# Kernel optimization log

Measured on AMD Instinct MI355X. Metric: run time of the kernel, lower is better.

The kernel has to match this reference:

```python
import jax, jax.numpy as jnp
import numpy as np

N_NODES = 100000
N_EDGES = 3200000
IN_DIM = 64
N_SEQ = 8
HID1 = 256
HID2 = 128
END = 64
OUT = 1


def _glorot(key, shape):
    fan_in, fan_out = shape
    lim = (6.0 / (fan_in + fan_out)) ** 0.5
    return jax.random.uniform(key, shape, jnp.float32, -lim, lim)


def setup_inputs() -> dict:
    key = jax.random.key(0)
    ks = jax.random.split(key, 10)
    features = jax.random.normal(ks[0], (N_NODES, IN_DIM, N_SEQ), jnp.float32)
    src = jax.random.randint(ks[1], (N_EDGES,), 0, N_NODES, jnp.int32)
    dst = jax.random.randint(ks[2], (N_EDGES,), 0, N_NODES, jnp.int32)
    return {
        "features": features,
        "src": src,
        "dst": dst,
        "W1": _glorot(ks[3], (IN_DIM * N_SEQ, HID1)),
        "b1": jnp.zeros((HID1,), jnp.float32),
        "W2": _glorot(ks[4], (HID1, HID2)),
        "b2": jnp.zeros((HID2,), jnp.float32),
        "Wo1": _glorot(ks[5], (HID2, END)),
        "bo1": jnp.zeros((END,), jnp.float32),
        "Wo2": _glorot(ks[6], (END, OUT)),
        "bo2": jnp.zeros((OUT,), jnp.float32),
    }


def _graph_conv(x, src, dst, W, b):
    # DGL GraphConv, norm='both': D_out^{-1/2} pre-scale, sum-aggregate, D_in^{-1/2} post-scale.
    n = x.shape[0]
    ones = jnp.ones((src.shape[0],), x.dtype)
    deg_out = jnp.clip(jax.ops.segment_sum(ones, src, num_segments=n), 1.0)
    deg_in = jnp.clip(jax.ops.segment_sum(ones, dst, num_segments=n), 1.0)
    x = x * jax.lax.rsqrt(deg_out)[:, None]
    # mult-first vs aggregate-first is mathematically identical; project to smaller dim first
    if W.shape[0] > W.shape[1]:
        x = x @ W
        agg = jax.ops.segment_sum(x[src], dst, num_segments=n)
    else:
        agg = jax.ops.segment_sum(x[src], dst, num_segments=n) @ W
    return agg * jax.lax.rsqrt(deg_in)[:, None] + b


def reference(features, src, dst, W1, b1, W2, b2, Wo1, bo1, Wo2, bo2):
    x = features.reshape(features.shape[0], IN_DIM * N_SEQ)  # [N, in_dim*n_seq]
    x = jax.nn.relu(_graph_conv(x, src, dst, W1, b1))
    x = _graph_conv(x, src, dst, W2, b2)
    x = jax.nn.relu(x @ Wo1 + bo1)
    return x @ Wo2 + bo2
```

## Files before the change

### kernel.cpp

```cpp
#include <hip/hip_runtime.h>
#include <hip/hip_bf16.h>
#include <hip/hip_fp16.h>

#define N_NODES 100000
#define N_EDGES 3200000
#define DIM0 512
#define DIM1 256
#define DIM2 128
#define DIM3 64
#define NSB 98

#define HPART 16384
#define NPARTS 7
#define HBLK 32

typedef _Float16 f16x8 __attribute__((ext_vector_type(8)));
typedef float f32x4 __attribute__((ext_vector_type(4)));


__global__ __launch_bounds__(256) void k_hist_lds(const int* __restrict__ src,
                                                  const int* __restrict__ dst,
                                                  int* __restrict__ cnt_out,
                                                  int* __restrict__ cnt_in) {
    __shared__ int h[HPART];
    int job = blockIdx.x / HBLK;
    int sub = blockIdx.x % HBLK;
    int arr = job / NPARTS;
    int part = job % NPARTS;
    int base = part * HPART;
    const int* __restrict__ keys = arr ? dst : src;
    int* __restrict__ cnt = arr ? cnt_in : cnt_out;

    for (int i = threadIdx.x; i < HPART; i += 256) h[i] = 0;
    __syncthreads();
    for (int e = sub * 256 + threadIdx.x; e < N_EDGES; e += HBLK * 256) {
        int k = keys[e] - base;
        if ((unsigned)k < (unsigned)HPART) atomicAdd(&h[k], 1);
    }
    __syncthreads();
    int lim = N_NODES - base; if (lim > HPART) lim = HPART;
    for (int i = threadIdx.x; i < lim; i += 256) {
        int v = h[i];
        if (v) atomicAdd(&cnt[base + i], v);
    }
}

__global__ __launch_bounds__(1024) void k_scan_a(const int* __restrict__ cnt,
                                                 int* __restrict__ excl,
                                                 int* __restrict__ bsum) {
    __shared__ int buf[1024];
    int tid = threadIdx.x;
    int i = blockIdx.x * 1024 + tid;
    int v = (i < N_NODES) ? cnt[i] : 0;
    buf[tid] = v;
    __syncthreads();
    #pragma unroll
    for (int off = 1; off < 1024; off <<= 1) {
        int t = (tid >= off) ? buf[tid - off] : 0;
        __syncthreads();
        buf[tid] += t;
        __syncthreads();
    }
    if (i < N_NODES) excl[i] = buf[tid] - v;
    if (tid == 1023) bsum[blockIdx.x] = buf[1023];
}

__global__ __launch_bounds__(128) void k_scan_b(const int* __restrict__ bsum,
                                                int* __restrict__ boff) {
    __shared__ int buf[128];
    int tid = threadIdx.x;
    int v = (tid < NSB) ? bsum[tid] : 0;
    buf[tid] = v;
    __syncthreads();
    #pragma unroll
    for (int off = 1; off < 128; off <<= 1) {
        int t = (tid >= off) ? buf[tid - off] : 0;
        __syncthreads();
        buf[tid] += t;
        __syncthreads();
    }
    if (tid < NSB) boff[tid] = buf[tid] - v;
    if (tid == 127) boff[NSB] = buf[127];
}

__global__ __launch_bounds__(256) void k_scan_c(const int* __restrict__ excl,
                                                const int* __restrict__ boff,
                                                const int* __restrict__ cnt_out,
                                                const int* __restrict__ cnt_in,
                                                int* __restrict__ row_ptr,
                                                int* __restrict__ cursor,
                                                float* __restrict__ s_out,
                                                float* __restrict__ s_in) {
    int i = blockIdx.x * 256 + threadIdx.x;
    if (i < N_NODES) {
        int rp = excl[i] + boff[i >> 10];
        row_ptr[i] = rp;
        cursor[i] = rp;
        int co = cnt_out[i]; if (co < 1) co = 1;
        int ci = cnt_in[i];  if (ci < 1) ci = 1;
        s_out[i] = rsqrtf((float)co);
        s_in[i]  = rsqrtf((float)ci);
    }
    if (i == 0) row_ptr[N_NODES] = boff[NSB];
}

__global__ __launch_bounds__(256) void k_scatter(const int* __restrict__ src,
                                                 const int* __restrict__ dst,
                                                 int* __restrict__ cursor,
                                                 int* __restrict__ esrc) {
    int e = blockIdx.x * 256 + threadIdx.x;
    if (e < N_EDGES) {
        int p = atomicAdd(&cursor[dst[e]], 1);
        esrc[p] = src[e];
    }
}


__global__ __launch_bounds__(256) void k_cvtW1(const float* __restrict__ W1,
                                               __half* __restrict__ W1t) {
    int idx = blockIdx.x * 256 + threadIdx.x;
    if (idx < DIM0 * DIM1) {
        int k = idx / DIM1, n = idx % DIM1;
        W1t[n * DIM0 + k] = __float2half(W1[idx]);
    }
}

__global__ __launch_bounds__(256) void k_cvtW2(const float* __restrict__ W2,
                                               __half* __restrict__ W2t) {
    int idx = blockIdx.x * 256 + threadIdx.x;
    if (idx < DIM1 * DIM2) {
        int k = idx / DIM2, n = idx % DIM2;
        W2t[n * DIM1 + k] = __float2half(W2[idx]);
    }
}


__global__ __launch_bounds__(256) void k_gemm1(const float* __restrict__ feat,
                                               const float* __restrict__ s_out,
                                               const __half* __restrict__ W1t,
                                               __half* __restrict__ y) {
    __shared__ __align__(16) _Float16 As[64][40];
    __shared__ __align__(16) _Float16 Bs[256][40];
    int tid = threadIdx.x;
    int wv = tid >> 6, lane = tid & 63;
    int m16 = lane & 15, quad = lane >> 4;
    int n0 = blockIdx.x * 64;

    int srow = tid >> 2;
    int scol = (tid & 3) * 8;
    int gr = n0 + srow;
    bool avalid = gr < N_NODES;
    int grc = avalid ? gr : (N_NODES - 1);
    float ascale = avalid ? s_out[gr] : 0.0f;
    const float* aptr = feat + (size_t)grc * DIM0 + scol;
    int bn = tid >> 2;
    int bc = (tid & 3) * 8;

    f32x4 acc[4][4] = {};
    for (int k0 = 0; k0 < DIM0; k0 += 32) {
        float4 f0 = *(const float4*)(aptr + k0);
        float4 f1 = *(const float4*)(aptr + k0 + 4);
        __syncthreads();
        {
            f16x8 h;
            h[0] = (_Float16)(f0.x * ascale); h[1] = (_Float16)(f0.y * ascale);
            h[2] = (_Float16)(f0.z * ascale); h[3] = (_Float16)(f0.w * ascale);
            h[4] = (_Float16)(f1.x * ascale); h[5] = (_Float16)(f1.y * ascale);
            h[6] = (_Float16)(f1.z * ascale); h[7] = (_Float16)(f1.w * ascale);
            *(f16x8*)&As[srow][scol] = h;
        }
        #pragma unroll
        for (int p = 0; p < 4; ++p) {
            int n = p * 64 + bn;
            f16x8 v = *(const f16x8*)(W1t + (size_t)n * DIM0 + k0 + bc);
            *(f16x8*)&Bs[n][bc] = v;
        }
        __syncthreads();
        f16x8 af[4], bf[4];
        #pragma unroll
        for (int r = 0; r < 4; ++r) af[r] = *(const f16x8*)&As[r * 16 + m16][quad * 8];
        #pragma unroll
        for (int c = 0; c < 4; ++c) bf[c] = *(const f16x8*)&Bs[wv * 64 + c * 16 + m16][quad * 8];
        #pragma unroll
        for (int r = 0; r < 4; ++r)
            #pragma unroll
            for (int c = 0; c < 4; ++c)
                acc[r][c] = __builtin_amdgcn_mfma_f32_16x16x32_f16(af[r], bf[c], acc[r][c], 0, 0, 0);
    }
    #pragma unroll
    for (int r = 0; r < 4; ++r) {
        #pragma unroll
        for (int i = 0; i < 4; ++i) {
            int row = n0 + r * 16 + quad * 4 + i;
            if (row < N_NODES) {
                #pragma unroll
                for (int c = 0; c < 4; ++c) {
                    int col = wv * 64 + c * 16 + m16;
                    y[(size_t)row * DIM1 + col] = __float2half(acc[r][c][i]);
                }
            }
        }
    }
}


__global__ __launch_bounds__(256) void k_agg256(const int* __restrict__ row_ptr,
                                                const int* __restrict__ esrc,
                                                const __half* __restrict__ y1,
                                                const float* __restrict__ s_in,
                                                const float* __restrict__ s_out,
                                                const float* __restrict__ b1,
                                                __half* __restrict__ x2) {
    int wave = threadIdx.x >> 6;
    int lane = threadIdx.x & 63;
    int n = blockIdx.x * 4 + wave;
    int beg = row_ptr[n], end = row_ptr[n + 1];
    const uint2* ybase = (const uint2*)y1;
    float4 acc = make_float4(0.f, 0.f, 0.f, 0.f);
    int i = beg;
    for (; i + 4 <= end; i += 4) {
        int s0 = esrc[i], s1 = esrc[i + 1], s2 = esrc[i + 2], s3 = esrc[i + 3];
        uint2 r0 = ybase[(size_t)s0 * 64 + lane];
        uint2 r1 = ybase[(size_t)s1 * 64 + lane];
        uint2 r2 = ybase[(size_t)s2 * 64 + lane];
        uint2 r3 = ybase[(size_t)s3 * 64 + lane];
        float2 a0 = __half22float2(*(__half2*)&r0.x), b0 = __half22float2(*(__half2*)&r0.y);
        float2 a1 = __half22float2(*(__half2*)&r1.x), b1v = __half22float2(*(__half2*)&r1.y);
        float2 a2 = __half22float2(*(__half2*)&r2.x), b2v = __half22float2(*(__half2*)&r2.y);
        float2 a3 = __half22float2(*(__half2*)&r3.x), b3v = __half22float2(*(__half2*)&r3.y);
        acc.x += a0.x + a1.x + a2.x + a3.x;
        acc.y += a0.y + a1.y + a2.y + a3.y;
        acc.z += b0.x + b1v.x + b2v.x + b3v.x;
        acc.w += b0.y + b1v.y + b2v.y + b3v.y;
    }
    for (; i < end; ++i) {
        uint2 r = ybase[(size_t)esrc[i] * 64 + lane];
        float2 a = __half22float2(*(__half2*)&r.x), b = __half22float2(*(__half2*)&r.y);
        acc.x += a.x; acc.y += a.y; acc.z += b.x; acc.w += b.y;
    }
    float si = s_in[n];
    float so = s_out[n];
    float4 bb = *(const float4*)&b1[lane * 4];
    acc.x = fmaxf(acc.x * si + bb.x, 0.f) * so;
    acc.y = fmaxf(acc.y * si + bb.y, 0.f) * so;
    acc.z = fmaxf(acc.z * si + bb.z, 0.f) * so;
    acc.w = fmaxf(acc.w * si + bb.w, 0.f) * so;
    union { uint2 u; __half2 h[2]; } cv;
    cv.h[0] = __floats2half2_rn(acc.x, acc.y);
    cv.h[1] = __floats2half2_rn(acc.z, acc.w);
    *(uint2*)&x2[(size_t)n * DIM1 + lane * 4] = cv.u;
}


__global__ __launch_bounds__(256) void k_gemm2(const __half* __restrict__ x2,
                                               const __half* __restrict__ W2t,
                                               __half* __restrict__ y) {
    __shared__ __align__(16) _Float16 As[64][40];
    __shared__ __align__(16) _Float16 Bs[128][40];
    int tid = threadIdx.x;
    int wv = tid >> 6, lane = tid & 63;
    int m16 = lane & 15, quad = lane >> 4;
    int n0 = blockIdx.x * 64;

    int srow = tid >> 2;
    int scol = (tid & 3) * 8;
    int gr = n0 + srow;
    int grc = (gr < N_NODES) ? gr : (N_NODES - 1);
    const __half* aptr = x2 + (size_t)grc * DIM1 + scol;
    int bn = tid >> 2;
    int bc = (tid & 3) * 8;

    f32x4 acc[4][2] = {};
    for (int k0 = 0; k0 < DIM1; k0 += 32) {
        f16x8 av = *(const f16x8*)(aptr + k0);
        __syncthreads();
        *(f16x8*)&As[srow][scol] = av;
        #pragma unroll
        for (int p = 0; p < 2; ++p) {
            int n = p * 64 + bn;
            f16x8 v = *(const f16x8*)(W2t + (size_t)n * DIM1 + k0 + bc);
            *(f16x8*)&Bs[n][bc] = v;
        }
        __syncthreads();
        f16x8 af[4], bf[2];
        #pragma unroll
        for (int r = 0; r < 4; ++r) af[r] = *(const f16x8*)&As[r * 16 + m16][quad * 8];
        #pragma unroll
        for (int c = 0; c < 2; ++c) bf[c] = *(const f16x8*)&Bs[wv * 32 + c * 16 + m16][quad * 8];
        #pragma unroll
        for (int r = 0; r < 4; ++r)
            #pragma unroll
            for (int c = 0; c < 2; ++c)
                acc[r][c] = __builtin_amdgcn_mfma_f32_16x16x32_f16(af[r], bf[c], acc[r][c], 0, 0, 0);
    }
    #pragma unroll
    for (int r = 0; r < 4; ++r) {
        #pragma unroll
        for (int i = 0; i < 4; ++i) {
            int row = n0 + r * 16 + quad * 4 + i;
            if (row < N_NODES) {
                #pragma unroll
                for (int c = 0; c < 2; ++c) {
                    int col = wv * 32 + c * 16 + m16;
                    y[(size_t)row * DIM2 + col] = __float2half(acc[r][c][i]);
                }
            }
        }
    }
}


__global__ __launch_bounds__(256) void k_agg_head(const int* __restrict__ row_ptr,
                                                  const int* __restrict__ esrc,
                                                  const __half* __restrict__ y2,
                                                  const float* __restrict__ s_in,
                                                  const float* __restrict__ b2,
                                                  const float* __restrict__ Wo1,
                                                  const float* __restrict__ bo1,
                                                  const float* __restrict__ Wo2,
                                                  const float* __restrict__ bo2,
                                                  float* __restrict__ out) {
    __shared__ float w1s[DIM2 * DIM3];
    __shared__ float w2s[DIM3];
    __shared__ float hs[4][DIM2];
    int tid = threadIdx.x;
    for (int i = tid; i < DIM2 * DIM3; i += 256) w1s[i] = Wo1[i];
    if (tid < DIM3) w2s[tid] = Wo2[tid];
    __syncthreads();

    int wave = tid >> 6, lane = tid & 63;
    int n = blockIdx.x * 4 + wave;
    int beg = row_ptr[n], end = row_ptr[n + 1];
    const unsigned* ybase = (const unsigned*)y2;
    float2 acc = make_float2(0.f, 0.f);
    int i = beg;
    for (; i + 4 <= end; i += 4) {
        unsigned r0 = ybase[(size_t)esrc[i] * 64 + lane];
        unsigned r1 = ybase[(size_t)esrc[i + 1] * 64 + lane];
        unsigned r2 = ybase[(size_t)esrc[i + 2] * 64 + lane];
        unsigned r3 = ybase[(size_t)esrc[i + 3] * 64 + lane];
        float2 f0 = __half22float2(*(__half2*)&r0);
        float2 f1 = __half22float2(*(__half2*)&r1);
        float2 f2 = __half22float2(*(__half2*)&r2);
        float2 f3 = __half22float2(*(__half2*)&r3);
        acc.x += f0.x + f1.x + f2.x + f3.x;
        acc.y += f0.y + f1.y + f2.y + f3.y;
    }
    for (; i < end; ++i) {
        unsigned r = ybase[(size_t)esrc[i] * 64 + lane];
        float2 f = __half22float2(*(__half2*)&r);
        acc.x += f.x; acc.y += f.y;
    }
    float si = s_in[n];
    float2 bv = *(const float2*)&b2[lane * 2];
    hs[wave][lane * 2 + 0] = acc.x * si + bv.x;
    hs[wave][lane * 2 + 1] = acc.y * si + bv.y;
    __syncthreads();

    float t = bo1[lane];
    #pragma unroll 8
    for (int k = 0; k < DIM2; ++k) t += hs[wave][k] * w1s[k * DIM3 + lane];
    t = fmaxf(t, 0.f);
    float p = t * w2s[lane];
    #pragma unroll
    for (int off = 32; off > 0; off >>= 1) p += __shfl_down(p, off);
    if (lane == 0) out[n] = p + bo2[0];
}


extern "C" void kernel_launch(void* const* d_in, const int* in_sizes, int n_in,
                              void* d_out, int out_size, void* d_ws, size_t ws_size,
                              hipStream_t stream) {
    const float* feat = (const float*)d_in[0];
    const int*   src  = (const int*)d_in[1];
    const int*   dst  = (const int*)d_in[2];
    const float* W1   = (const float*)d_in[3];
    const float* b1   = (const float*)d_in[4];
    const float* W2   = (const float*)d_in[5];
    const float* b2   = (const float*)d_in[6];
    const float* Wo1  = (const float*)d_in[7];
    const float* bo1  = (const float*)d_in[8];
    const float* Wo2  = (const float*)d_in[9];
    const float* bo2  = (const float*)d_in[10];
    float* out = (float*)d_out;

    char* ws = (char*)d_ws;
    size_t off = 0;
    auto alloc = [&](size_t bytes) -> char* {
        char* p = ws + off;
        off = (off + bytes + 255) & ~(size_t)255;
        return p;
    };
    int*    cnt_out = (int*)alloc(N_NODES * 4);
    int*    cnt_in  = (int*)alloc(N_NODES * 4);
    int*    row_ptr = (int*)alloc((N_NODES + 1) * 4);
    int*    cursor  = (int*)alloc(N_NODES * 4);
    int*    excl    = (int*)alloc(N_NODES * 4);
    int*    bsum    = (int*)alloc((NSB + 1) * 4);
    int*    boff    = (int*)alloc((NSB + 1) * 4);
    int*    esrc    = (int*)alloc((size_t)N_EDGES * 4);
    float*  s_out   = (float*)alloc(N_NODES * 4);
    float*  s_in    = (float*)alloc(N_NODES * 4);
    __half* W1t     = (__half*)alloc((size_t)DIM0 * DIM1 * 2);
    __half* W2t     = (__half*)alloc((size_t)DIM1 * DIM2 * 2);
    __half* y1h     = (__half*)alloc((size_t)N_NODES * DIM1 * 2);
    __half* x2h     = (__half*)alloc((size_t)N_NODES * DIM1 * 2);
    __half* y2h     = (__half*)alloc((size_t)N_NODES * DIM2 * 2);

    hipMemsetAsync(cnt_out, 0, N_NODES * 4, stream);
    hipMemsetAsync(cnt_in, 0, N_NODES * 4, stream);

    k_hist_lds<<<2 * NPARTS * HBLK, 256, 0, stream>>>(src, dst, cnt_out, cnt_in);
    k_scan_a<<<NSB, 1024, 0, stream>>>(cnt_in, excl, bsum);
    k_scan_b<<<1, 128, 0, stream>>>(bsum, boff);
    k_scan_c<<<(N_NODES + 255) / 256, 256, 0, stream>>>(excl, boff, cnt_out, cnt_in,
                                                        row_ptr, cursor, s_out, s_in);
    k_scatter<<<(N_EDGES + 255) / 256, 256, 0, stream>>>(src, dst, cursor, esrc);

    k_cvtW1<<<(DIM0 * DIM1 + 255) / 256, 256, 0, stream>>>(W1, W1t);
    k_cvtW2<<<(DIM1 * DIM2 + 255) / 256, 256, 0, stream>>>(W2, W2t);

    int nblk = (N_NODES + 63) / 64;
    k_gemm1<<<nblk, 256, 0, stream>>>(feat, s_out, W1t, y1h);
    k_agg256<<<N_NODES / 4, 256, 0, stream>>>(row_ptr, esrc, y1h, s_in, s_out, b1, x2h);
    k_gemm2<<<nblk, 256, 0, stream>>>(x2h, W2t, y2h);
    k_agg_head<<<N_NODES / 4, 256, 0, stream>>>(row_ptr, esrc, y2h, s_in, b2,
                                                Wo1, bo1, Wo2, bo2, out);
}
```

Before: 1.283 ms.

## Replace global-atomic CSR scatter with per-slice LDS histograms and local offsets

The degree histogram now writes a private 16-bit-packed histogram per edge slice and partition, and a reduce kernel sums them. While reducing the in-degree histograms it also stores an exclusive prefix per slice back into the same buffer. The scatter kernel then builds per-slice base offsets in LDS and uses shared-memory atomics instead of global atomics on a cursor array. This removes the memsets, the cursor array and the contended global atomics, at the cost of extra histogram traffic and of each block scanning its whole edge slice once per partition. The head's Wo1 weights are also packed as half2 in LDS, which halves that footprint but rounds the weights to fp16.

```diff
diff --git a/kernel.cpp b/kernel.cpp
--- a/kernel.cpp
+++ b/kernel.cpp
@@ -11,38 +11,57 @@
 #define NSB 98
 
 #define HPART 16384
-#define NPARTS 7
-#define HBLK 32
+#define HPAIR 8192
+#define NP 7
+#define NSL 32
+#define SLC (N_EDGES / NSL)
 
 typedef _Float16 f16x8 __attribute__((ext_vector_type(8)));
 typedef float f32x4 __attribute__((ext_vector_type(4)));
 
 
-__global__ __launch_bounds__(256) void k_hist_lds(const int* __restrict__ src,
-                                                  const int* __restrict__ dst,
-                                                  int* __restrict__ cnt_out,
-                                                  int* __restrict__ cnt_in) {
-    __shared__ int h[HPART];
-    int job = blockIdx.x / HBLK;
-    int sub = blockIdx.x % HBLK;
-    int arr = job / NPARTS;
-    int part = job % NPARTS;
+__global__ __launch_bounds__(256) void k_hist_priv(const int* __restrict__ src,
+                                                   const int* __restrict__ dst,
+                                                   unsigned* __restrict__ hp) {
+    __shared__ unsigned h32[HPAIR];
+    int blk = blockIdx.x, part = blockIdx.y, arr = blockIdx.z;
+    const int* __restrict__ keys = arr ? dst : src;
     int base = part * HPART;
-    const int* __restrict__ keys = arr ? dst : src;
-    int* __restrict__ cnt = arr ? cnt_in : cnt_out;
-
-    for (int i = threadIdx.x; i < HPART; i += 256) h[i] = 0;
-    __syncthreads();
-    for (int e = sub * 256 + threadIdx.x; e < N_EDGES; e += HBLK * 256) {
+    for (int i = threadIdx.x; i < HPAIR; i += 256) h32[i] = 0;
+    __syncthreads();
+    int e0 = blk * SLC, e1 = e0 + SLC;
+    for (int e = e0 + threadIdx.x; e < e1; e += 256) {
         int k = keys[e] - base;
-        if ((unsigned)k < (unsigned)HPART) atomicAdd(&h[k], 1);
-    }
-    __syncthreads();
-    int lim = N_NODES - base; if (lim > HPART) lim = HPART;
-    for (int i = threadIdx.x; i < lim; i += 256) {
-        int v = h[i];
-        if (v) atomicAdd(&cnt[base + i], v);
-    }
+        if ((unsigned)k < (unsigned)HPART)
+            atomicAdd(&h32[k >> 1], 1u << ((k & 1) * 16));
+    }
+    __syncthreads();
+    unsigned* out = hp + ((size_t)(arr * NP + part) * NSL + blk) * HPAIR;
+    for (int i = threadIdx.x; i < HPAIR; i += 256) out[i] = h32[i];
+}
+
+__global__ __launch_bounds__(256) void k_reduce(unsigned* __restrict__ hp,
+                                                int* __restrict__ cnt_out,
+                                                int* __restrict__ cnt_in) {
+    int idx = blockIdx.x * 256 + threadIdx.x;
+    if (idx >= 2 * NP * HPAIR) return;
+    int arr = idx / (NP * HPAIR);
+    int rem = idx % (NP * HPAIR);
+    int part = rem / HPAIR;
+    int j = rem % HPAIR;
+    unsigned* p = hp + ((size_t)(arr * NP + part) * NSL) * HPAIR + j;
+    unsigned lo = 0, hi = 0;
+    #pragma unroll 8
+    for (int b = 0; b < NSL; ++b) {
+        unsigned v = p[(size_t)b * HPAIR];
+        if (arr == 1) p[(size_t)b * HPAIR] = (lo & 0xffffu) | (hi << 16);
+        lo += v & 0xffffu;
+        hi += v >> 16;
+    }
+    int node0 = part * HPART + 2 * j;
+    int* cnt = arr ? cnt_in : cnt_out;
+    if (node0 < N_NODES) cnt[node0] = (int)lo;
+    if (node0 + 1 < N_NODES) cnt[node0 + 1] = (int)hi;
 }
 
 __global__ __launch_bounds__(1024) void k_scan_a(const int* __restrict__ cnt,
@@ -88,14 +107,11 @@
                                                 const int* __restrict__ cnt_out,
                                                 const int* __restrict__ cnt_in,
                                                 int* __restrict__ row_ptr,
-                                                int* __restrict__ cursor,
                                                 float* __restrict__ s_out,
                                                 float* __restrict__ s_in) {
     int i = blockIdx.x * 256 + threadIdx.x;
     if (i < N_NODES) {
-        int rp = excl[i] + boff[i >> 10];
-        row_ptr[i] = rp;
-        cursor[i] = rp;
+        row_ptr[i] = excl[i] + boff[i >> 10];
         int co = cnt_out[i]; if (co < 1) co = 1;
         int ci = cnt_in[i];  if (ci < 1) ci = 1;
         s_out[i] = rsqrtf((float)co);
@@ -104,14 +120,31 @@
     if (i == 0) row_ptr[N_NODES] = boff[NSB];
 }
 
-__global__ __launch_bounds__(256) void k_scatter(const int* __restrict__ src,
-                                                 const int* __restrict__ dst,
-                                                 int* __restrict__ cursor,
-                                                 int* __restrict__ esrc) {
-    int e = blockIdx.x * 256 + threadIdx.x;
-    if (e < N_EDGES) {
-        int p = atomicAdd(&cursor[dst[e]], 1);
-        esrc[p] = src[e];
+__global__ __launch_bounds__(256) void k_scatter_nr(const int* __restrict__ src,
+                                                    const int* __restrict__ dst,
+                                                    const int* __restrict__ row_ptr,
+                                                    const unsigned* __restrict__ hp,
+                                                    int* __restrict__ esrc) {
+    __shared__ int base_s[HPART];
+    int blk = blockIdx.x, part = blockIdx.y;
+    int pbase = part * HPART;
+    const unsigned* off_p = hp + ((size_t)(1 * NP + part) * NSL + blk) * HPAIR;
+    for (int k = threadIdx.x; k < HPART; k += 256) {
+        int node = pbase + k;
+        int rp = (node < N_NODES) ? row_ptr[node] : 0;
+        unsigned w = off_p[k >> 1];
+        unsigned off = (k & 1) ? (w >> 16) : (w & 0xffffu);
+        base_s[k] = rp + (int)off;
+    }
+    __syncthreads();
+    int e0 = blk * SLC, e1 = e0 + SLC;
+    for (int e = e0 + threadIdx.x; e < e1; e += 256) {
+        int d = dst[e];
+        int k = d - pbase;
+        if ((unsigned)k < (unsigned)HPART) {
+            int p = atomicAdd(&base_s[k], 1);
+            esrc[p] = src[e];
+        }
     }
 }
 
@@ -320,11 +353,14 @@
                                                   const float* __restrict__ Wo2,
                                                   const float* __restrict__ bo2,
                                                   float* __restrict__ out) {
-    __shared__ float w1s[DIM2 * DIM3];
+    __shared__ __half2 w1p[DIM2 / 2][DIM3];
     __shared__ float w2s[DIM3];
     __shared__ float hs[4][DIM2];
     int tid = threadIdx.x;
-    for (int i = tid; i < DIM2 * DIM3; i += 256) w1s[i] = Wo1[i];
+    for (int i = tid; i < (DIM2 / 2) * DIM3; i += 256) {
+        int m = i >> 6, l = i & 63;
+        w1p[m][l] = __floats2half2_rn(Wo1[(2 * m) * DIM3 + l], Wo1[(2 * m + 1) * DIM3 + l]);
+    }
     if (tid < DIM3) w2s[tid] = Wo2[tid];
     __syncthreads();
 
@@ -359,7 +395,11 @@
 
     float t = bo1[lane];
     #pragma unroll 8
-    for (int k = 0; k < DIM2; ++k) t += hs[wave][k] * w1s[k * DIM3 + lane];
+    for (int m = 0; m < DIM2 / 2; ++m) {
+        float2 h2 = *(const float2*)&hs[wave][2 * m];
+        float2 wf = __half22float2(w1p[m][lane]);
+        t += h2.x * wf.x + h2.y * wf.y;
+    }
     t = fmaxf(t, 0.f);
     float p = t * w2s[lane];
     #pragma unroll
@@ -391,31 +431,29 @@
         off = (off + bytes + 255) & ~(size_t)255;
         return p;
     };
-    int*    cnt_out = (int*)alloc(N_NODES * 4);
-    int*    cnt_in  = (int*)alloc(N_NODES * 4);
-    int*    row_ptr = (int*)alloc((N_NODES + 1) * 4);
-    int*    cursor  = (int*)alloc(N_NODES * 4);
-    int*    excl    = (int*)alloc(N_NODES * 4);
-    int*    bsum    = (int*)alloc((NSB + 1) * 4);
-    int*    boff    = (int*)alloc((NSB + 1) * 4);
-    int*    esrc    = (int*)alloc((size_t)N_EDGES * 4);
-    float*  s_out   = (float*)alloc(N_NODES * 4);
-    float*  s_in    = (float*)alloc(N_NODES * 4);
-    __half* W1t     = (__half*)alloc((size_t)DIM0 * DIM1 * 2);
-    __half* W2t     = (__half*)alloc((size_t)DIM1 * DIM2 * 2);
-    __half* y1h     = (__half*)alloc((size_t)N_NODES * DIM1 * 2);
-    __half* x2h     = (__half*)alloc((size_t)N_NODES * DIM1 * 2);
-    __half* y2h     = (__half*)alloc((size_t)N_NODES * DIM2 * 2);
-
-    hipMemsetAsync(cnt_out, 0, N_NODES * 4, stream);
-    hipMemsetAsync(cnt_in, 0, N_NODES * 4, stream);
-
-    k_hist_lds<<<2 * NPARTS * HBLK, 256, 0, stream>>>(src, dst, cnt_out, cnt_in);
+    int*      cnt_out = (int*)alloc(N_NODES * 4);
+    int*      cnt_in  = (int*)alloc(N_NODES * 4);
+    int*      row_ptr = (int*)alloc((N_NODES + 1) * 4);
+    int*      excl    = (int*)alloc(N_NODES * 4);
+    int*      bsum    = (int*)alloc((NSB + 1) * 4);
+    int*      boff    = (int*)alloc((NSB + 1) * 4);
+    int*      esrc    = (int*)alloc((size_t)N_EDGES * 4);
+    unsigned* histp   = (unsigned*)alloc((size_t)2 * NP * NSL * HPAIR * 4);
+    float*    s_out   = (float*)alloc(N_NODES * 4);
+    float*    s_in    = (float*)alloc(N_NODES * 4);
+    __half*   W1t     = (__half*)alloc((size_t)DIM0 * DIM1 * 2);
+    __half*   W2t     = (__half*)alloc((size_t)DIM1 * DIM2 * 2);
+    __half*   y1h     = (__half*)alloc((size_t)N_NODES * DIM1 * 2);
+    __half*   x2h     = (__half*)alloc((size_t)N_NODES * DIM1 * 2);
+    __half*   y2h     = (__half*)alloc((size_t)N_NODES * DIM2 * 2);
+
+    k_hist_priv<<<dim3(NSL, NP, 2), 256, 0, stream>>>(src, dst, histp);
+    k_reduce<<<(2 * NP * HPAIR + 255) / 256, 256, 0, stream>>>(histp, cnt_out, cnt_in);
     k_scan_a<<<NSB, 1024, 0, stream>>>(cnt_in, excl, bsum);
     k_scan_b<<<1, 128, 0, stream>>>(bsum, boff);
     k_scan_c<<<(N_NODES + 255) / 256, 256, 0, stream>>>(excl, boff, cnt_out, cnt_in,
-                                                        row_ptr, cursor, s_out, s_in);
-    k_scatter<<<(N_EDGES + 255) / 256, 256, 0, stream>>>(src, dst, cursor, esrc);
+                                                        row_ptr, s_out, s_in);
+    k_scatter_nr<<<dim3(NSL, NP), 256, 0, stream>>>(src, dst, row_ptr, histp, esrc);
 
     k_cvtW1<<<(DIM0 * DIM1 + 255) / 256, 256, 0, stream>>>(W1, W1t);
     k_cvtW2<<<(DIM1 * DIM2 + 255) / 256, 256, 0, stream>>>(W2, W2t);
```

Result: faster. 1.166 ms (-9.1%).
